# Kernel tuning notes

Measured on AMD Instinct MI355X. Metric: run time of the kernel, lower is better.

## Reference

```python
import jax, jax.numpy as jnp
import numpy as np

N = 65536      # number of nodes being updated
EMBED = 1024   # embed_size
G = 256        # g_size (per-head dim)
MLP = 256      # mlp_size
H = 4          # n_head


def setup_inputs() -> dict:
    key = jax.random.key(0)
    ks = jax.random.split(key, 8)
    s_in = 1.0 / np.sqrt(EMBED)
    s_g = 1.0 / np.sqrt(G)
    s_m = 1.0 / np.sqrt(MLP)
    s_hg = 1.0 / np.sqrt(H * G)
    return {
        "q": jax.random.normal(ks[0], (N, EMBED), jnp.float32),
        "rep": jax.random.normal(ks[1], (N, EMBED), jnp.float32),
        "Wq": jax.random.normal(ks[2], (EMBED, H * G), jnp.float32) * s_in,
        "Wk": jax.random.normal(ks[3], (EMBED, H * G), jnp.float32) * s_in,
        "Wv": jax.random.normal(ks[4], (EMBED, H * G), jnp.float32) * s_in,
        "W1": jax.random.normal(ks[5], (H, G, MLP), jnp.float32) * s_g,
        "b1": jnp.zeros((H, MLP), jnp.float32),
        "W2": jax.random.normal(ks[6], (H, MLP, G), jnp.float32) * s_m,
        "b2": jnp.zeros((H, G), jnp.float32),
        "Ws": jax.random.normal(ks[7], (H * G, EMBED), jnp.float32) * s_hg,
    }


def reference(q, rep, Wq, Wk, Wv, W1, b1, W2, b2, Ws):
    # Per-head Q/K/V projections: [N, E] -> [N, H, G]
    n = q.shape[0]
    Qh = (q @ Wq).reshape(n, H, G)
    Kh = (rep @ Wk).reshape(n, H, G)
    Vh = (rep @ Wv).reshape(n, H, G)
    # Elementwise scaled attention gate (Q, K are per-node vectors -> 2D attn)
    gate = jax.nn.sigmoid(Qh * Kh * (1.0 / np.sqrt(G)))
    z = gate * Vh  # [N, H, G]
    # Per-head MLP (num_mlp = 1 block): G -> MLP -> G with ReLU
    h1 = jax.nn.relu(jnp.einsum('nhg,hgm->nhm', z, W1) + b1)
    z2 = jnp.einsum('nhm,hmg->nhg', h1, W2) + b2
    update_gate = z2.reshape(n, H * G)
    # update_attn_scale (no bias) + fused residual: h = Q - K + proj(gate)
    h = q - rep + update_gate @ Ws
    return h
```

## Files before the change

kernel.cpp:

```cpp
#include <hip/hip_runtime.h>
#include <hip/hip_bf16.h>


typedef __attribute__((ext_vector_type(8))) short bf16x8;
typedef __attribute__((ext_vector_type(4))) float f32x4;
typedef __attribute__((ext_vector_type(4))) short short4v;

static __device__ __forceinline__ short f2b(float x) {
  __hip_bfloat16 h = __float2bfloat16(x);
  return __builtin_bit_cast(short, h);
}
static __device__ __forceinline__ float b2f(short s) {
  unsigned u = ((unsigned)(unsigned short)s) << 16;
  return __builtin_bit_cast(float, u);
}

static __device__ __forceinline__ void stage_half(
    const short* __restrict__ g, long ld, short* dst, int wave, int lane)
{
  const int rw = lane >> 2;
  const int gg = (lane & 3) ^ ((rw >> 1) & 3);
  const short* gl = g + (long)rw * ld + (gg << 3);
  #pragma unroll
  for (int j = 0; j < 2; ++j) {
    const int r0 = j * 128 + wave * 16;
    __builtin_amdgcn_global_load_lds(
        (const __attribute__((address_space(1))) void*)(gl + (long)r0 * ld),
        (__attribute__((address_space(3))) void*)(dst + r0 * 32),
        16, 0, 0);
  }
}

__global__ void cvt_bf16(const float* __restrict__ in, short* __restrict__ out, long n) {
  long i = ((long)blockIdx.x * blockDim.x + threadIdx.x) * 4;
  const long stride = (long)gridDim.x * blockDim.x * 4;
  for (; i < n; i += stride) {
    float4 v = *(const float4*)(in + i);
    short4v o = { f2b(v.x), f2b(v.y), f2b(v.z), f2b(v.w) };
    *(short4v*)(out + i) = o;
  }
}

__global__ void prep_weights(
    const float* __restrict__ Wq, const float* __restrict__ Wk, const float* __restrict__ Wv,
    const float* __restrict__ W1, const float* __restrict__ W2, const float* __restrict__ Ws,
    short* __restrict__ wqt, short* __restrict__ wkt, short* __restrict__ wvt,
    short* __restrict__ w1t, short* __restrict__ w2t, short* __restrict__ wst)
{
  const int job = blockIdx.z;
  const float* src; short* dst; int R, C;
  if (job < 3)       { src = (job==0)?Wq:((job==1)?Wk:Wv); dst = (job==0)?wqt:((job==1)?wkt:wvt); R = 1024; C = 1024; }
  else if (job == 3) { src = Ws; dst = wst; R = 1024; C = 1024; }
  else if (job < 8)  { int h = job-4; src = W1 + h*65536; dst = w1t + h*65536; R = 256; C = 256; }
  else               { int h = job-8; src = W2 + h*65536; dst = w2t + h*65536; R = 256; C = 256; }
  const int c0 = blockIdx.x * 32, r0 = blockIdx.y * 32;
  if (c0 >= C || r0 >= R) return;
  __shared__ float t[32][33];
  for (int i = threadIdx.y; i < 32; i += 8)
    t[i][threadIdx.x] = src[(long)(r0 + i) * C + c0 + threadIdx.x];
  __syncthreads();
  for (int i = threadIdx.y; i < 32; i += 8)
    dst[(long)(c0 + i) * R + r0 + threadIdx.x] = f2b(t[threadIdx.x][i]);
}

template <int KDIM, int GATE, bool RELU, bool BIAS, bool RESID, bool SWZ>
__global__ __launch_bounds__(512, 2) void gemm_bf16(
    const short* __restrict__ A, long lda, long zsa,
    const short* __restrict__ Bt, long ldb, long zsb,
    void* __restrict__ outv, long ldc, long zsc,
    const float* __restrict__ bias, long zsbias,
    const short* __restrict__ eg,
    const float* __restrict__ q, const float* __restrict__ rep)
{
  __shared__ __align__(16) short lA[2][2][8192];
  __shared__ __align__(16) short lB[2][2][8192];
  const int lane = threadIdx.x & 63, wave = threadIdx.x >> 6;
  const int wm = wave >> 2, wn = wave & 3;
  int bx = blockIdx.x, by = blockIdx.y;
  if (SWZ) {
    const int nbx = gridDim.x;
    const int flat = by * nbx + bx;
    const int chunk = (int)(gridDim.x * gridDim.y) >> 3;
    const int fid = (flat & 7) * chunk + (flat >> 3);
    bx = fid % nbx; by = fid / nbx;
  }
  const long bm = (long)by * 256;
  const int  bn = bx * 256;
  const int  zi = blockIdx.z;

  const short* Ab = A + (long)zi * zsa + bm * lda;
  const short* Bb = Bt + (long)zi * zsb + (long)bn * ldb;
  constexpr int NT = KDIM / 64;
  const int g0 = lane >> 4;
  const int arow = wm * 128 + (lane & 15);
  const int bcol = wn * 64 + (lane & 15);

  auto stA = [&](int buf, int ks, int t) {
    const int tc = t < NT ? t : NT - 1;
    stage_half(Ab + tc * 64 + ks * 32, lda, &lA[buf][ks][0], wave, lane);
  };
  auto stB = [&](int buf, int ks, int t) {
    const int tc = t < NT ? t : NT - 1;
    stage_half(Bb + tc * 64 + ks * 32, ldb, &lB[buf][ks][0], wave, lane);
  };

  stA(0, 0, 0); stB(0, 0, 0); stA(0, 1, 0); stB(0, 1, 0);
  stA(1, 0, 1); stB(1, 0, 1);
  asm volatile("s_waitcnt vmcnt(4)" ::: "memory");
  __builtin_amdgcn_s_barrier();

  f32x4 acc[8][4] = {};
  bf16x8 b[4];

#define PHASE(BUF, MH, KS, LOADB, STAGE_STMT, CHECK)                        \
  {                                                                         \
    const short* aS = &lA[BUF][KS][0];                                      \
    const short* bS = &lB[BUF][KS][0];                                      \
    if (LOADB) {                                                            \
      _Pragma("unroll")                                                     \
      for (int j = 0; j < 4; ++j) {                                         \
        const int c = bcol + j * 16;                                        \
        b[j] = *(const bf16x8*)(bS + c * 32 + (((g0 ^ (c >> 1)) & 3) << 3));\
      }                                                                     \
    }                                                                       \
    bf16x8 a[4];                                                            \
    _Pragma("unroll")                                                       \
    for (int i2 = 0; i2 < 4; ++i2) {                                        \
      const int r = arow + (MH) * 64 + i2 * 16;                             \
      a[i2] = *(const bf16x8*)(aS + r * 32 + (((g0 ^ (r >> 1)) & 3) << 3)); \
    }                                                                       \
    STAGE_STMT;                                                             \
    if (CHECK) asm volatile("s_waitcnt vmcnt(4)" ::: "memory");             \
    asm volatile("" ::: "memory");                                          \
    __builtin_amdgcn_s_barrier();                                           \
    asm volatile("s_waitcnt lgkmcnt(0)" ::: "memory");                      \
    __builtin_amdgcn_sched_barrier(0);                                      \
    __builtin_amdgcn_s_setprio(1);                                          \
    _Pragma("unroll")                                                       \
    for (int i2 = 0; i2 < 4; ++i2)                                          \
      _Pragma("unroll")                                                     \
      for (int j = 0; j < 4; ++j)                                           \
        acc[(MH) * 4 + i2][j] = __builtin_amdgcn_mfma_f32_16x16x32_bf16(    \
            a[i2], b[j], acc[(MH) * 4 + i2][j], 0, 0, 0);                   \
    __builtin_amdgcn_s_setprio(0);                                          \
    asm volatile("" ::: "memory");                                          \
    __builtin_amdgcn_s_barrier();                                           \
  }

  for (int t = 0; t < NT; t += 2) {
    PHASE(0, 0, 0, true,  stA(1, 1, t + 1), false)
    PHASE(0, 1, 0, false, stB(1, 1, t + 1), false)
    PHASE(0, 0, 1, true,  stA(0, 0, t + 2), false)
    PHASE(0, 1, 1, false, stB(0, 0, t + 2), true)
    PHASE(1, 0, 0, true,  stA(0, 1, t + 2), false)
    PHASE(1, 1, 0, false, stB(0, 1, t + 2), false)
    PHASE(1, 0, 1, true,  stA(1, 0, t + 3), false)
    PHASE(1, 1, 1, false, stB(1, 0, t + 3), true)
  }
#undef PHASE

  #pragma unroll
  for (int i = 0; i < 8; ++i)
    #pragma unroll
    for (int j = 0; j < 4; ++j)
      #pragma unroll
      for (int r = 0; r < 4; ++r) {
        const int rl = wm * 128 + i * 16 + ((lane >> 4) << 2) + r;
        const int cl = wn * 64 + j * 16 + (lane & 15);
        float v = acc[i][j][r];
        if (BIAS) v += bias[(long)zi * zsbias + bn + cl];
        if (RELU) v = v > 0.0f ? v : 0.0f;
        const long row = bm + rl;
        const long gi = (long)zi * zsc + row * ldc + bn + cl;
        if (GATE == 1) {
          const float x = b2f(eg[gi]) * v * 0.0625f;
          v = 1.0f / (1.0f + __expf(-x));
        } else if (GATE == 2) {
          v = b2f(eg[gi]) * v;
        }
        if (RESID) {
          ((float*)outv)[gi] = q[gi] - rep[gi] + v;
        } else {
          ((short*)outv)[gi] = f2b(v);
        }
      }
}

extern "C" void kernel_launch(void* const* d_in, const int* in_sizes, int n_in,
                              void* d_out, int out_size, void* d_ws, size_t ws_size,
                              hipStream_t stream) {
  const float* q   = (const float*)d_in[0];
  const float* rep = (const float*)d_in[1];
  const float* Wq  = (const float*)d_in[2];
  const float* Wk  = (const float*)d_in[3];
  const float* Wv  = (const float*)d_in[4];
  const float* W1  = (const float*)d_in[5];
  const float* b1  = (const float*)d_in[6];
  const float* W2  = (const float*)d_in[7];
  const float* b2  = (const float*)d_in[8];
  const float* Ws  = (const float*)d_in[9];
  float* out = (float*)d_out;

  const long NE = 67108864L;
  char* ws = (char*)d_ws;
  short* qb  = (short*)(ws);
  short* rb  = (short*)(ws + NE * 2);
  short* gh  = (short*)(ws + NE * 4);
  short* zb  = qb;
  short* ugb = rb;
  short* h1b = gh;
  char*  wp  = ws + NE * 6;
  short* wqt = (short*)(wp);
  short* wkt = (short*)(wp + 2097152);
  short* wvt = (short*)(wp + 4194304);
  short* wst = (short*)(wp + 6291456);
  short* w1t = (short*)(wp + 8388608);
  short* w2t = (short*)(wp + 8912896);

  cvt_bf16<<<4096, 256, 0, stream>>>(q,   qb, NE);
  cvt_bf16<<<4096, 256, 0, stream>>>(rep, rb, NE);
  prep_weights<<<dim3(32, 32, 12), dim3(32, 8), 0, stream>>>(
      Wq, Wk, Wv, W1, W2, Ws, wqt, wkt, wvt, w1t, w2t, wst);

  gemm_bf16<1024, 0, false, false, false, true><<<dim3(4, 256), 512, 0, stream>>>(
      qb, 1024, 0, wqt, 1024, 0, gh, 1024, 0, nullptr, 0, nullptr, nullptr, nullptr);
  gemm_bf16<1024, 1, false, false, false, true><<<dim3(4, 256), 512, 0, stream>>>(
      rb, 1024, 0, wkt, 1024, 0, gh, 1024, 0, nullptr, 0, gh, nullptr, nullptr);
  gemm_bf16<1024, 2, false, false, false, true><<<dim3(4, 256), 512, 0, stream>>>(
      rb, 1024, 0, wvt, 1024, 0, zb, 1024, 0, nullptr, 0, gh, nullptr, nullptr);

  gemm_bf16<256, 0, true, true, false, false><<<dim3(1, 256, 4), 512, 0, stream>>>(
      zb, 1024, 256, w1t, 256, 65536, h1b, 1024, 256, b1, 256, nullptr, nullptr, nullptr);
  gemm_bf16<256, 0, false, true, false, false><<<dim3(1, 256, 4), 512, 0, stream>>>(
      h1b, 1024, 256, w2t, 256, 65536, ugb, 1024, 256, b2, 256, nullptr, nullptr, nullptr);
  gemm_bf16<1024, 0, false, false, true, true><<<dim3(4, 256), 512, 0, stream>>>(
      ugb, 1024, 0, wst, 1024, 0, out, 1024, 0, nullptr, 0, nullptr, q, rep);
}
```

Baseline: 1.113 ms.

## Fuse K and V projections into one GEMM with gated epilogue; bf16 residual

Adds a dedicated kernel that computes the K and V projections together from a single staged tile of rep, applying the sigmoid gate and V product in the epilogue. This removes one full pass over rep and the intermediate gate write/read to gh. The final residual now reads the bf16 copies of q and rep instead of the fp32 originals, which halves that traffic but lowers the precision of the residual term. A separate z buffer is added to the workspace so rb and qb stay live.

```diff
diff --git a/kernel.cpp b/kernel.cpp
--- a/kernel.cpp
+++ b/kernel.cpp
@@ -29,6 +29,18 @@
         (__attribute__((address_space(3))) void*)(dst + r0 * 32),
         16, 0, 0);
   }
+}
+
+static __device__ __forceinline__ void stage_half128(
+    const short* __restrict__ g, long ld, short* dst, int wave, int lane)
+{
+  const int rw = lane >> 2;
+  const int gg = (lane & 3) ^ ((rw >> 1) & 3);
+  const int r0 = wave * 16;
+  __builtin_amdgcn_global_load_lds(
+      (const __attribute__((address_space(1))) void*)(g + (long)(r0 + rw) * ld + (gg << 3)),
+      (__attribute__((address_space(3))) void*)(dst + r0 * 32),
+      16, 0, 0);
 }
 
 __global__ void cvt_bf16(const float* __restrict__ in, short* __restrict__ out, long n) {
@@ -63,14 +75,13 @@
     dst[(long)(c0 + i) * R + r0 + threadIdx.x] = f2b(t[threadIdx.x][i]);
 }
 
-template <int KDIM, int GATE, bool RELU, bool BIAS, bool RESID, bool SWZ>
+template <int KDIM, bool RELU, bool BIAS, bool RESID, bool SWZ>
 __global__ __launch_bounds__(512, 2) void gemm_bf16(
     const short* __restrict__ A, long lda, long zsa,
     const short* __restrict__ Bt, long ldb, long zsb,
     void* __restrict__ outv, long ldc, long zsc,
     const float* __restrict__ bias, long zsbias,
-    const short* __restrict__ eg,
-    const float* __restrict__ q, const float* __restrict__ rep)
+    const short* __restrict__ qres, const short* __restrict__ rres)
 {
   __shared__ __align__(16) short lA[2][2][8192];
   __shared__ __align__(16) short lB[2][2][8192];
@@ -172,17 +183,130 @@
         if (RELU) v = v > 0.0f ? v : 0.0f;
         const long row = bm + rl;
         const long gi = (long)zi * zsc + row * ldc + bn + cl;
-        if (GATE == 1) {
-          const float x = b2f(eg[gi]) * v * 0.0625f;
-          v = 1.0f / (1.0f + __expf(-x));
-        } else if (GATE == 2) {
-          v = b2f(eg[gi]) * v;
-        }
         if (RESID) {
-          ((float*)outv)[gi] = q[gi] - rep[gi] + v;
+          ((float*)outv)[gi] = b2f(qres[gi]) - b2f(rres[gi]) + v;
         } else {
           ((short*)outv)[gi] = f2b(v);
         }
+      }
+}
+
+__global__ __launch_bounds__(512, 2) void gemm_g23(
+    const short* __restrict__ rb,
+    const short* __restrict__ wkt,
+    const short* __restrict__ wvt,
+    const short* __restrict__ gh,
+    short* __restrict__ zb)
+{
+  __shared__ __align__(16) short lA[2][2][8192];
+  __shared__ __align__(16) short lK[2][2][4096];
+  __shared__ __align__(16) short lV[2][2][4096];
+  const int lane = threadIdx.x & 63, wave = threadIdx.x >> 6;
+  const int wm = wave >> 2, wn = wave & 3;
+  int bx = blockIdx.x, by = blockIdx.y;
+  {
+    const int flat = by * 8 + bx;
+    const int chunk = (int)(gridDim.x * gridDim.y) >> 3;
+    const int fid = (flat & 7) * chunk + (flat >> 3);
+    bx = fid & 7; by = fid >> 3;
+  }
+  const long bm = (long)by * 256;
+  const int  bn = bx * 128;
+
+  const short* Ab = rb + bm * 1024;
+  const short* Kb = wkt + (long)bn * 1024;
+  const short* Vb = wvt + (long)bn * 1024;
+  constexpr int NT = 16;
+  const int g0 = lane >> 4;
+  const int arow = wm * 128 + (lane & 15);
+  const int bcol = wn * 32 + (lane & 15);
+
+  auto stA = [&](int buf, int ks, int t) {
+    const int tc = t < NT ? t : NT - 1;
+    stage_half(Ab + tc * 64 + ks * 32, 1024, &lA[buf][ks][0], wave, lane);
+  };
+  auto stK = [&](int buf, int ks, int t) {
+    const int tc = t < NT ? t : NT - 1;
+    stage_half128(Kb + tc * 64 + ks * 32, 1024, &lK[buf][ks][0], wave, lane);
+  };
+  auto stV = [&](int buf, int ks, int t) {
+    const int tc = t < NT ? t : NT - 1;
+    stage_half128(Vb + tc * 64 + ks * 32, 1024, &lV[buf][ks][0], wave, lane);
+  };
+
+  stA(0, 0, 0); stK(0, 0, 0); stV(0, 0, 0);
+  stA(0, 1, 0); stK(0, 1, 0); stV(0, 1, 0);
+  stA(1, 0, 1); stK(1, 0, 1); stV(1, 0, 1);
+  asm volatile("s_waitcnt vmcnt(4)" ::: "memory");
+  __builtin_amdgcn_s_barrier();
+
+  f32x4 ack[8][2] = {};
+  f32x4 acv[8][2] = {};
+  bf16x8 bk[2], bv[2];
+
+#define PHASEG(BUF, MH, KS, LOADB, STAGE_STMT, CHECK)                       \
+  {                                                                         \
+    const short* aS = &lA[BUF][KS][0];                                      \
+    if (LOADB) {                                                            \
+      _Pragma("unroll")                                                     \
+      for (int j = 0; j < 2; ++j) {                                         \
+        const int c = bcol + j * 16;                                        \
+        const int so = c * 32 + (((g0 ^ (c >> 1)) & 3) << 3);               \
+        bk[j] = *(const bf16x8*)(&lK[BUF][KS][0] + so);                     \
+        bv[j] = *(const bf16x8*)(&lV[BUF][KS][0] + so);                     \
+      }                                                                     \
+    }                                                                       \
+    bf16x8 a[4];                                                            \
+    _Pragma("unroll")                                                       \
+    for (int i2 = 0; i2 < 4; ++i2) {                                        \
+      const int r = arow + (MH) * 64 + i2 * 16;                             \
+      a[i2] = *(const bf16x8*)(aS + r * 32 + (((g0 ^ (r >> 1)) & 3) << 3)); \
+    }                                                                       \
+    STAGE_STMT;                                                             \
+    if (CHECK) asm volatile("s_waitcnt vmcnt(4)" ::: "memory");             \
+    asm volatile("" ::: "memory");                                          \
+    __builtin_amdgcn_s_barrier();                                           \
+    asm volatile("s_waitcnt lgkmcnt(0)" ::: "memory");                      \
+    __builtin_amdgcn_sched_barrier(0);                                      \
+    __builtin_amdgcn_s_setprio(1);                                          \
+    _Pragma("unroll")                                                       \
+    for (int i2 = 0; i2 < 4; ++i2)                                          \
+      _Pragma("unroll")                                                     \
+      for (int j = 0; j < 2; ++j) {                                         \
+        ack[(MH) * 4 + i2][j] = __builtin_amdgcn_mfma_f32_16x16x32_bf16(    \
+            a[i2], bk[j], ack[(MH) * 4 + i2][j], 0, 0, 0);                  \
+        acv[(MH) * 4 + i2][j] = __builtin_amdgcn_mfma_f32_16x16x32_bf16(    \
+            a[i2], bv[j], acv[(MH) * 4 + i2][j], 0, 0, 0);                  \
+      }                                                                     \
+    __builtin_amdgcn_s_setprio(0);                                          \
+    asm volatile("" ::: "memory");                                          \
+    __builtin_amdgcn_s_barrier();                                           \
+  }
+
+  for (int t = 0; t < NT; t += 2) {
+    PHASEG(0, 0, 0, true,  stA(1, 1, t + 1), false)
+    PHASEG(0, 1, 0, false, { stK(1, 1, t + 1); stV(1, 1, t + 1); }, false)
+    PHASEG(0, 0, 1, true,  stA(0, 0, t + 2), false)
+    PHASEG(0, 1, 1, false, { stK(0, 0, t + 2); stV(0, 0, t + 2); }, true)
+    PHASEG(1, 0, 0, true,  stA(0, 1, t + 2), false)
+    PHASEG(1, 1, 0, false, { stK(0, 1, t + 2); stV(0, 1, t + 2); }, false)
+    PHASEG(1, 0, 1, true,  stA(1, 0, t + 3), false)
+    PHASEG(1, 1, 1, false, { stK(1, 0, t + 3); stV(1, 0, t + 3); }, true)
+  }
+#undef PHASEG
+
+  #pragma unroll
+  for (int i = 0; i < 8; ++i)
+    #pragma unroll
+    for (int j = 0; j < 2; ++j)
+      #pragma unroll
+      for (int r = 0; r < 4; ++r) {
+        const int rl = wm * 128 + i * 16 + ((lane >> 4) << 2) + r;
+        const int cl = wn * 32 + j * 16 + (lane & 15);
+        const long gi = (bm + rl) * 1024 + bn + cl;
+        const float x = b2f(gh[gi]) * ack[i][j][r] * 0.0625f;
+        const float gate = 1.0f / (1.0f + __expf(-x));
+        zb[gi] = f2b(gate * acv[i][j][r]);
       }
 }
 
@@ -206,10 +330,10 @@
   short* qb  = (short*)(ws);
   short* rb  = (short*)(ws + NE * 2);
   short* gh  = (short*)(ws + NE * 4);
-  short* zb  = qb;
-  short* ugb = rb;
+  short* zb  = (short*)(ws + NE * 6);
   short* h1b = gh;
-  char*  wp  = ws + NE * 6;
+  short* ugb = zb;
+  char*  wp  = ws + NE * 8;
   short* wqt = (short*)(wp);
   short* wkt = (short*)(wp + 2097152);
   short* wvt = (short*)(wp + 4194304);
@@ -222,17 +346,14 @@
   prep_weights<<<dim3(32, 32, 12), dim3(32, 8), 0, stream>>>(
       Wq, Wk, Wv, W1, W2, Ws, wqt, wkt, wvt, w1t, w2t, wst);
 
-  gemm_bf16<1024, 0, false, false, false, true><<<dim3(4, 256), 512, 0, stream>>>(
-      qb, 1024, 0, wqt, 1024, 0, gh, 1024, 0, nullptr, 0, nullptr, nullptr, nullptr);
-  gemm_bf16<1024, 1, false, false, false, true><<<dim3(4, 256), 512, 0, stream>>>(
-      rb, 1024, 0, wkt, 1024, 0, gh, 1024, 0, nullptr, 0, gh, nullptr, nullptr);
-  gemm_bf16<1024, 2, false, false, false, true><<<dim3(4, 256), 512, 0, stream>>>(
-      rb, 1024, 0, wvt, 1024, 0, zb, 1024, 0, nullptr, 0, gh, nullptr, nullptr);
-
-  gemm_bf16<256, 0, true, true, false, false><<<dim3(1, 256, 4), 512, 0, stream>>>(
-      zb, 1024, 256, w1t, 256, 65536, h1b, 1024, 256, b1, 256, nullptr, nullptr, nullptr);
-  gemm_bf16<256, 0, false, true, false, false><<<dim3(1, 256, 4), 512, 0, stream>>>(
-      h1b, 1024, 256, w2t, 256, 65536, ugb, 1024, 256, b2, 256, nullptr, nullptr, nullptr);
-  gemm_bf16<1024, 0, false, false, true, true><<<dim3(4, 256), 512, 0, stream>>>(
-      ugb, 1024, 0, wst, 1024, 0, out, 1024, 0, nullptr, 0, nullptr, q, rep);
-}
+  gemm_bf16<1024, false, false, false, true><<<dim3(4, 256), 512, 0, stream>>>(
+      qb, 1024, 0, wqt, 1024, 0, gh, 1024, 0, nullptr, 0, nullptr, nullptr);
+  gemm_g23<<<dim3(8, 256), 512, 0, stream>>>(rb, wkt, wvt, gh, zb);
+
+  gemm_bf16<256, true, true, false, false><<<dim3(1, 256, 4), 512, 0, stream>>>(
+      zb, 1024, 256, w1t, 256, 65536, h1b, 1024, 256, b1, 256, nullptr, nullptr);
+  gemm_bf16<256, false, true, false, false><<<dim3(1, 256, 4), 512, 0, stream>>>(
+      h1b, 1024, 256, w2t, 256, 65536, ugb, 1024, 256, b2, 256, nullptr, nullptr);
+  gemm_bf16<1024, false, false, true, true><<<dim3(4, 256), 512, 0, stream>>>(
+      ugb, 1024, 0, wst, 1024, 0, out, 1024, 0, nullptr, 0, qb, rb);
+}
```

New measurement: 1.044 ms. 1.07x faster.
